# Kernel tuning notes

Measured on AMD Instinct MI355X. Metric: run time of the kernel, lower is better.

Reference implementation:

```python
import jax, jax.numpy as jnp
import numpy as np
import math

D_MODEL = 2048
N_HEADS = 16
D_HEAD = D_MODEL // N_HEADS

def setup_inputs() -> dict:
    key = jax.random.key(0)
    ks = jax.random.split(key, 6)
    B, S, D = 4, 2048, D_MODEL
    scale = 1.0 / math.sqrt(D)
    x  = jax.random.normal(ks[0], (B, S, D), dtype=jnp.float32)
    Wq = jax.random.normal(ks[1], (D, D), dtype=jnp.float32) * scale
    Wk = jax.random.normal(ks[2], (D, D), dtype=jnp.float32) * scale
    Wv = jax.random.normal(ks[3], (D, D), dtype=jnp.float32) * scale
    Wo = jax.random.normal(ks[4], (D, D), dtype=jnp.float32) * scale
    bo = jax.random.normal(ks[5], (D,), dtype=jnp.float32) * 0.01
    return {"x": x, "Wq": Wq, "Wk": Wk, "Wv": Wv, "Wo": Wo, "bo": bo}

def reference(x, Wq, Wk, Wv, Wo, bo):
    B, S, D = x.shape
    H, Dh = N_HEADS, D_HEAD
    # projections (bias=False for q/k/v); torch Linear: y = x @ W^T
    q = (x @ Wq.T).reshape(B, S, H, Dh).transpose(0, 2, 1, 3)  # [B,H,S,Dh]
    k = (x @ Wk.T).reshape(B, S, H, Dh).transpose(0, 2, 1, 3)
    v = (x @ Wv.T).reshape(B, S, H, Dh).transpose(0, 2, 1, 3)
    scores = jnp.einsum('bhqd,bhkd->bhqk', q, k) / math.sqrt(Dh)  # [B,H,S,S]
    causal = jnp.tril(jnp.ones((S, S), dtype=bool))
    scores = jnp.where(causal, scores, -jnp.inf)
    attn = jax.nn.softmax(scores, axis=-1)
    # dropout p=0.0 -> identity (eval)
    out = jnp.einsum('bhqk,bhkd->bhqd', attn, v)  # [B,H,S,Dh]
    out = out.transpose(0, 2, 1, 3).reshape(B, S, D)
    return out @ Wo.T + bo
```

## Files before the change

kernel.cpp:

```cpp
#include <hip/hip_runtime.h>
#include <stdint.h>

#define D_MODEL 2048
#define NH 16
#define DH 128
#define BATCH 4
#define SEQ 2048
#define MTOT (BATCH*SEQ)
#define LDQ 6144

typedef __bf16 bf16x8 __attribute__((ext_vector_type(8)));
typedef float f32x4 __attribute__((ext_vector_type(4)));
typedef short short8 __attribute__((ext_vector_type(8)));

static __device__ __forceinline__ unsigned short f2bf(float f) {
  union { float f; unsigned int u; } v; v.f = f;
  return (unsigned short)((v.u + 0x7FFFu + ((v.u >> 16) & 1u)) >> 16);
}

#define FENCEM() asm volatile("" ::: "memory")
#define GBAR() do { FENCEM(); __builtin_amdgcn_s_barrier(); FENCEM(); } while (0)

__global__ __launch_bounds__(256) void cvt_all_k(const float* __restrict__ x,
                                                 const float* __restrict__ w0, const float* __restrict__ w1,
                                                 const float* __restrict__ w2, const float* __restrict__ w3,
                                                 unsigned short* __restrict__ xo,
                                                 unsigned short* __restrict__ wo_cat,
                                                 unsigned short* __restrict__ wo_o) {
  const size_t WSZ = (size_t)D_MODEL * D_MODEL;
  int id = blockIdx.x;
  const float* src; unsigned short* dst; int lo;
  if (id < 8192) { src = x; dst = xo; lo = id; }
  else {
    int wsel = (id - 8192) >> 11;
    lo = (id - 8192) & 2047;
    switch (wsel) {
      case 0: src = w0; dst = wo_cat; break;
      case 1: src = w1; dst = wo_cat + WSZ; break;
      case 2: src = w2; dst = wo_cat + 2 * WSZ; break;
      default: src = w3; dst = wo_o; break;
    }
  }
  int i = (lo * 256 + threadIdx.x) * 8;
  float4 a = *(const float4*)(src + i);
  float4 b = *(const float4*)(src + i + 4);
  union { unsigned short u[8]; short8 v; } o;
  o.u[0] = f2bf(a.x); o.u[1] = f2bf(a.y); o.u[2] = f2bf(a.z); o.u[3] = f2bf(a.w);
  o.u[4] = f2bf(b.x); o.u[5] = f2bf(b.y); o.u[6] = f2bf(b.z); o.u[7] = f2bf(b.w);
  *(short8*)(dst + i) = o.v;
}

template<bool OUT_BF16, bool ADD_BIAS>
__global__ __launch_bounds__(512, 2) void gemm256(const unsigned short* __restrict__ A,
                                                  const unsigned short* __restrict__ B,
                                                  void* __restrict__ C,
                                                  const float* __restrict__ bias,
                                                  int M, int N, int K) {
  __shared__ __align__(16) unsigned short As[2][256 * 64];
  __shared__ __align__(16) unsigned short Bs[2][256 * 64];

  const int tid = threadIdx.x;
  const int lane = tid & 63;
  const int l15 = lane & 15, l4 = lane >> 4;
  const int wid = tid >> 6;
  const int wr = wid >> 2, wc = wid & 3;

  const int gx = gridDim.x;
  const int id = blockIdx.y * gx + blockIdx.x;
  const int msl = gx >> 2;
  const int nsl = gridDim.y >> 1;
  const int xcd = id & 7;
  const int lid = id >> 3;
  const int bm = (xcd >> 1) * msl + lid / nsl;
  const int bn = (xcd & 1) * nsl + lid % nsl;

  const int NT = K >> 6;

  const int st_r = tid >> 3;
  const int st_c = (tid & 7) ^ (st_r & 7);
  const int st_ld = st_r * 64 + (tid & 7) * 8;

#define STAGE_A(t, h) do { \
  const int _b = (t) & 1; \
  _Pragma("unroll") \
  for (int _i = 0; _i < 2; ++_i) { \
    const unsigned short* _g = A + (size_t)(bm * 256 + (h) * 128 + _i * 64 + st_r) * K + (t) * 64 + st_c * 8; \
    __builtin_amdgcn_global_load_lds((const __attribute__((address_space(1))) void*)_g, \
        (__attribute__((address_space(3))) void*)(&As[_b][(h) * 8192 + _i * 4096 + st_ld]), 16, 0, 0); \
  } \
} while (0)

#define STAGE_B(t, h) do { \
  const int _b = (t) & 1; \
  _Pragma("unroll") \
  for (int _i = 0; _i < 2; ++_i) { \
    const unsigned short* _g = B + (size_t)(bn * 256 + (h) * 128 + _i * 64 + st_r) * K + (t) * 64 + st_c * 8; \
    __builtin_amdgcn_global_load_lds((const __attribute__((address_space(1))) void*)_g, \
        (__attribute__((address_space(3))) void*)(&Bs[_b][(h) * 8192 + _i * 4096 + st_ld]), 16, 0, 0); \
  } \
} while (0)

#define LDA_F(dst, bufb, mh) do { \
  _Pragma("unroll") \
  for (int _mi = 0; _mi < 4; ++_mi) { \
    int _row = wr * 128 + (mh) * 64 + _mi * 16 + l15; \
    _Pragma("unroll") \
    for (int _kk = 0; _kk < 2; ++_kk) \
      dst[_mi][_kk] = *(const bf16x8*)&As[bufb][_row * 64 + ((_kk * 4 + l4) ^ (l15 & 7)) * 8]; \
  } \
} while (0)

#define LDB_F(dst, bufb, nq) do { \
  _Pragma("unroll") \
  for (int _ni = 0; _ni < 2; ++_ni) { \
    int _row = wc * 64 + (nq) * 32 + _ni * 16 + l15; \
    _Pragma("unroll") \
    for (int _kk = 0; _kk < 2; ++_kk) \
      dst[_ni][_kk] = *(const bf16x8*)&Bs[bufb][_row * 64 + ((_kk * 4 + l4) ^ (l15 & 7)) * 8]; \
  } \
} while (0)

#define PHASE_MFMA(MH, NQ, BFR) do { \
  _Pragma("unroll") \
  for (int _mi = 0; _mi < 4; ++_mi) { \
    _Pragma("unroll") \
    for (int _ni = 0; _ni < 2; ++_ni) { \
      acc[(MH) * 4 + _mi][(NQ) * 2 + _ni] = __builtin_amdgcn_mfma_f32_16x16x32_bf16( \
          af[_mi][0], BFR[_ni][0], acc[(MH) * 4 + _mi][(NQ) * 2 + _ni], 0, 0, 0); \
      acc[(MH) * 4 + _mi][(NQ) * 2 + _ni] = __builtin_amdgcn_mfma_f32_16x16x32_bf16( \
          af[_mi][1], BFR[_ni][1], acc[(MH) * 4 + _mi][(NQ) * 2 + _ni], 0, 0, 0); \
    } \
  } \
} while (0)

  f32x4 acc[8][4] = {};

  STAGE_A(0, 0); STAGE_A(0, 1);
  STAGE_B(0, 0); STAGE_B(0, 1);
  if (NT > 1) { STAGE_A(1, 0); STAGE_A(1, 1); }
  if (NT > 1) asm volatile("s_waitcnt vmcnt(4)" ::: "memory");
  else        asm volatile("s_waitcnt vmcnt(0)" ::: "memory");
  GBAR();

  for (int t = 0; t < NT; ++t) {
    const int bufb = t & 1;
    bf16x8 af[4][2], bf0[2][2], bf1[2][2];

    LDA_F(af, bufb, 0);
    LDB_F(bf0, bufb, 0);
    LDB_F(bf1, bufb, 1);
    if (t + 1 < NT) { STAGE_B(t + 1, 0); STAGE_B(t + 1, 1); }
    __builtin_amdgcn_s_setprio(1);
    PHASE_MFMA(0, 0, bf0);
    PHASE_MFMA(0, 1, bf1);
    __builtin_amdgcn_s_setprio(0);

    LDA_F(af, bufb, 1);
    asm volatile("s_waitcnt lgkmcnt(0)" ::: "memory");
    GBAR();

    if (t + 2 < NT) { STAGE_A(t + 2, 0); STAGE_A(t + 2, 1); }
    __builtin_amdgcn_s_setprio(1);
    PHASE_MFMA(1, 1, bf1);
    PHASE_MFMA(1, 0, bf0);
    __builtin_amdgcn_s_setprio(0);
    if (t + 2 < NT) asm volatile("s_waitcnt vmcnt(4)" ::: "memory");
    else            asm volatile("s_waitcnt vmcnt(0)" ::: "memory");
    GBAR();
  }

  const int row0 = bm * 256 + wr * 128;
  const int col0 = bn * 256 + wc * 64;
#pragma unroll
  for (int mi = 0; mi < 8; ++mi) {
#pragma unroll
    for (int ni = 0; ni < 4; ++ni) {
      int col = col0 + ni * 16 + l15;
#pragma unroll
      for (int r = 0; r < 4; ++r) {
        int row = row0 + mi * 16 + l4 * 4 + r;
        float v = acc[mi][ni][r];
        if (ADD_BIAS) v += bias[col];
        if (OUT_BF16)
          ((unsigned short*)C)[(size_t)row * N + col] = f2bf(v);
        else
          ((float*)C)[(size_t)row * N + col] = v;
      }
    }
  }
#undef STAGE_A
#undef STAGE_B
#undef LDA_F
#undef LDB_F
#undef PHASE_MFMA
}

__global__ __launch_bounds__(256, 2) void attn_k(const unsigned short* __restrict__ Qp,
                                                 const unsigned short* __restrict__ Kp,
                                                 const unsigned short* __restrict__ Vp,
                                                 unsigned short* __restrict__ O) {
  __shared__ __align__(16) unsigned short Ks[2][64 * 128];
  __shared__ __align__(16) unsigned short Vt[2][128 * 64];
  __shared__ __align__(16) unsigned int   Pl[4][32 * 32];

  const int tid = threadIdx.x;
  const int lane = tid & 63;
  const int l15 = lane & 15, l4 = lane >> 4;
  const int w = tid >> 6;

  const int idx = blockIdx.y * gridDim.x + blockIdx.x;
  const int x8 = idx & 7, j = idx >> 3;
  const int bh = x8 * 8 + (j & 7);
  const int qt = 15 - (j >> 3);
  const int b = bh >> 4, h = bh & 15;

  const size_t baseI = (size_t)b * SEQ * LDQ + (size_t)h * DH;
  const size_t baseO = (size_t)b * SEQ * D_MODEL + (size_t)h * DH;
  const int qw = qt * 128 + w * 32;

  bf16x8 qf[2][4];
#pragma unroll
  for (int qg = 0; qg < 2; ++qg) {
    const unsigned short* qptr = Qp + baseI + (size_t)(qw + qg * 16 + l15) * LDQ;
#pragma unroll
    for (int kk = 0; kk < 4; ++kk)
      qf[qg][kk] = *(const bf16x8*)(qptr + kk * 32 + l4 * 8);
  }

  f32x4 acc[2][8] = {};
  float m_run[2] = {-3.4028235e38f, -3.4028235e38f};
  float lp[2] = {0.f, 0.f};
  const float SC = 0.12751743f;

  short8 vreg[4];
  const int nkt = 2 * qt + 2;

  const int vkp0 = tid >> 4, vch0 = tid & 15;
  const int vkp1 = (tid + 256) >> 4, vch1 = vch0;

#pragma unroll
  for (int it = 0; it < 4; ++it) {
    int c = tid + it * 256;
    int key = c >> 4, pos = c & 15;
    int gchunk = pos ^ (key & 7);
    const unsigned short* ga = Kp + baseI + (size_t)key * LDQ + gchunk * 8;
    __builtin_amdgcn_global_load_lds((const __attribute__((address_space(1))) void*)ga,
                                     (__attribute__((address_space(3))) void*)(&Ks[0][c * 8]),
                                     16, 0, 0);
  }
  FENCEM();
  {
    const unsigned short* gv0 = Vp + baseI + (size_t)(2 * vkp0) * LDQ + vch0 * 8;
    vreg[0] = *(const short8*)(gv0);
    vreg[1] = *(const short8*)(gv0 + LDQ);
    const unsigned short* gv1 = Vp + baseI + (size_t)(2 * vkp1) * LDQ + vch1 * 8;
    vreg[2] = *(const short8*)(gv1);
    vreg[3] = *(const short8*)(gv1 + LDQ);
  }

  for (int kt = 0; kt < nkt; ++kt) {
    const int cur = kt & 1;
    const int kv0 = kt * 64;
    const bool act = (kv0 <= qw + 31);

    asm volatile("s_waitcnt vmcnt(4)" ::: "memory");
    GBAR();

    f32x4 sacc[2][4] = {};
    if (act) {
      __builtin_amdgcn_s_setprio(1);
#pragma unroll
      for (int st = 0; st < 4; ++st) {
        int key = st * 16 + l15;
#pragma unroll
        for (int kk = 0; kk < 4; ++kk) {
          bf16x8 kf = *(const bf16x8*)&Ks[cur][key * 128 + ((kk * 32 + l4 * 8) ^ ((key & 7) << 3))];
          sacc[0][st] = __builtin_amdgcn_mfma_f32_16x16x32_bf16(kf, qf[0][kk], sacc[0][st], 0, 0, 0);
          sacc[1][st] = __builtin_amdgcn_mfma_f32_16x16x32_bf16(kf, qf[1][kk], sacc[1][st], 0, 0, 0);
        }
      }
      __builtin_amdgcn_s_setprio(0);
    }
    FENCEM();

    if (kt + 1 < nkt) {
      const int kn0 = kv0 + 64;
      const int nb = cur ^ 1;
#pragma unroll
      for (int it = 0; it < 4; ++it) {
        int c = tid + it * 256;
        int key = c >> 4, pos = c & 15;
        int gchunk = pos ^ (key & 7);
        const unsigned short* ga = Kp + baseI + (size_t)(kn0 + key) * LDQ + gchunk * 8;
        __builtin_amdgcn_global_load_lds((const __attribute__((address_space(1))) void*)ga,
                                         (__attribute__((address_space(3))) void*)(&Ks[nb][c * 8]),
                                         16, 0, 0);
      }
      asm volatile("s_waitcnt vmcnt(4)" ::: "memory");
    } else {
      asm volatile("s_waitcnt vmcnt(0)" ::: "memory");
    }

#pragma unroll
    for (int i = 0; i < 2; ++i) {
      int kp = i ? vkp1 : vkp0;
      int ch = i ? vch1 : vch0;
      union { short8 v; unsigned short u[8]; } ua, ub;
      ua.v = vreg[2 * i]; ub.v = vreg[2 * i + 1];
#pragma unroll
      for (int j2 = 0; j2 < 8; ++j2) {
        int dh = ch * 8 + j2;
        int sv = (ch ^ j2) & 7;
        unsigned val = (unsigned)ua.u[j2] | ((unsigned)ub.u[j2] << 16);
        *(unsigned int*)&Vt[cur][dh * 64 + ((2 * kp) ^ (sv << 3))] = val;
      }
    }
    if (kt + 1 < nkt) {
      const int kn0 = kv0 + 64;
      const unsigned short* gv0 = Vp + baseI + (size_t)(kn0 + 2 * vkp0) * LDQ + vch0 * 8;
      vreg[0] = *(const short8*)(gv0);
      vreg[1] = *(const short8*)(gv0 + LDQ);
      const unsigned short* gv1 = Vp + baseI + (size_t)(kn0 + 2 * vkp1) * LDQ + vch1 * 8;
      vreg[2] = *(const short8*)(gv1);
      vreg[3] = *(const short8*)(gv1 + LDQ);
    }
    __syncthreads();

    if (act) {
      const bool tail = (kv0 + 63 > qw);
      float tmax[2];
#pragma unroll
      for (int qg = 0; qg < 2; ++qg) {
        if (tail) {
          int q = qw + qg * 16 + l15;
#pragma unroll
          for (int st = 0; st < 4; ++st)
#pragma unroll
            for (int r = 0; r < 4; ++r) {
              int key = kv0 + st * 16 + l4 * 4 + r;
              if (key > q) sacc[qg][st][r] = -3.0e38f;
            }
        }
        float a0 = fmaxf(fmaxf(sacc[qg][0][0], sacc[qg][0][1]), fmaxf(sacc[qg][0][2], sacc[qg][0][3]));
        float a1 = fmaxf(fmaxf(sacc[qg][1][0], sacc[qg][1][1]), fmaxf(sacc[qg][1][2], sacc[qg][1][3]));
        float a2 = fmaxf(fmaxf(sacc[qg][2][0], sacc[qg][2][1]), fmaxf(sacc[qg][2][2], sacc[qg][2][3]));
        float a3 = fmaxf(fmaxf(sacc[qg][3][0], sacc[qg][3][1]), fmaxf(sacc[qg][3][2], sacc[qg][3][3]));
        float t = fmaxf(fmaxf(a0, a1), fmaxf(a2, a3));
        t = fmaxf(t, __shfl_xor(t, 16));
        t = fmaxf(t, __shfl_xor(t, 32));
        tmax[qg] = t;
      }
      bool grow = (tmax[0] > m_run[0] + 8.f) || (tmax[1] > m_run[1] + 8.f);
      if (__any(grow)) {
#pragma unroll
        for (int qg = 0; qg < 2; ++qg) {
          float nm = fmaxf(m_run[qg], tmax[qg]);
          float scl = __builtin_amdgcn_exp2f((m_run[qg] - nm) * SC);
          m_run[qg] = nm;
          lp[qg] *= scl;
#pragma unroll
          for (int r = 0; r < 4; ++r) {
            float srow = __shfl(scl, l4 * 4 + r);
#pragma unroll
            for (int df = 0; df < 8; ++df) acc[qg][df][r] *= srow;
          }
        }
      }
#pragma unroll
      for (int qg = 0; qg < 2; ++qg) {
        int q = qg * 16 + l15;
        float ps = 0.f;
#pragma unroll
        for (int st = 0; st < 4; ++st) {
          float p0 = __builtin_amdgcn_exp2f((sacc[qg][st][0] - m_run[qg]) * SC);
          float p1 = __builtin_amdgcn_exp2f((sacc[qg][st][1] - m_run[qg]) * SC);
          float p2 = __builtin_amdgcn_exp2f((sacc[qg][st][2] - m_run[qg]) * SC);
          float p3 = __builtin_amdgcn_exp2f((sacc[qg][st][3] - m_run[qg]) * SC);
          ps += (p0 + p1) + (p2 + p3);
          unsigned w0 = (unsigned)f2bf(p0) | ((unsigned)f2bf(p1) << 16);
          unsigned w1 = (unsigned)f2bf(p2) | ((unsigned)f2bf(p3) << 16);
          int kw0 = st * 8 + l4 * 2;
          Pl[w][q * 32 + (kw0 ^ ((q & 7) << 2))] = w0;
          Pl[w][q * 32 + ((kw0 + 1) ^ ((q & 7) << 2))] = w1;
        }
        lp[qg] += ps;
      }
      __builtin_amdgcn_s_setprio(1);
#pragma unroll
      for (int ks2 = 0; ks2 < 2; ++ks2) {
        int kwb = ks2 * 16 + l4 * 4;
        bf16x8 pa0 = *(const bf16x8*)&Pl[w][l15 * 32 + (kwb ^ ((l15 & 7) << 2))];
        bf16x8 pa1 = *(const bf16x8*)&Pl[w][(16 + l15) * 32 + (kwb ^ ((l15 & 7) << 2))];
#pragma unroll
        for (int df = 0; df < 8; ++df) {
          int dh = df * 16 + l15;
          int sv = ((dh >> 3) ^ dh) & 7;
          bf16x8 vb = *(const bf16x8*)&Vt[cur][dh * 64 + ((ks2 * 32 + l4 * 8) ^ (sv << 3))];
          acc[0][df] = __builtin_amdgcn_mfma_f32_16x16x32_bf16(pa0, vb, acc[0][df], 0, 0, 0);
          acc[1][df] = __builtin_amdgcn_mfma_f32_16x16x32_bf16(pa1, vb, acc[1][df], 0, 0, 0);
        }
      }
      __builtin_amdgcn_s_setprio(0);
    }
  }

#pragma unroll
  for (int qg = 0; qg < 2; ++qg) {
    float t = lp[qg];
    t += __shfl_xor(t, 16);
    t += __shfl_xor(t, 32);
    float linv = 1.0f / t;
#pragma unroll
    for (int r = 0; r < 4; ++r) {
      float lrow = __shfl(linv, l4 * 4 + r);
      int row = qw + qg * 16 + l4 * 4 + r;
#pragma unroll
      for (int df = 0; df < 8; ++df)
        O[baseO + (size_t)row * D_MODEL + df * 16 + l15] = f2bf(acc[qg][df][r] * lrow);
    }
  }
}

extern "C" void kernel_launch(void* const* d_in, const int* in_sizes, int n_in,
                              void* d_out, int out_size, void* d_ws, size_t ws_size,
                              hipStream_t stream) {
  const float* x  = (const float*)d_in[0];
  const float* Wq = (const float*)d_in[1];
  const float* Wk = (const float*)d_in[2];
  const float* Wv = (const float*)d_in[3];
  const float* Wo = (const float*)d_in[4];
  const float* bo = (const float*)d_in[5];
  float* out = (float*)d_out;

  unsigned short* ws = (unsigned short*)d_ws;
  const size_t XSZ = (size_t)MTOT * D_MODEL;
  const size_t WSZ = (size_t)D_MODEL * D_MODEL;
  unsigned short* xb   = ws;
  unsigned short* Wcat = xb + XSZ;
  unsigned short* Wob  = Wcat + 3 * WSZ;
  unsigned short* QKV  = Wob + WSZ;
  unsigned short* AOb  = xb;

  cvt_all_k<<<16384, 256, 0, stream>>>(x, Wq, Wk, Wv, Wo, xb, Wcat, Wob);

  dim3 gq(MTOT / 256, LDQ / 256);
  gemm256<true, false><<<gq, 512, 0, stream>>>(xb, Wcat, QKV, nullptr, MTOT, LDQ, D_MODEL);

  dim3 ga(SEQ / 128, BATCH * NH);
  attn_k<<<ga, 256, 0, stream>>>(QKV, QKV + 2048, QKV + 4096, AOb);

  dim3 gg(MTOT / 256, D_MODEL / 256);
  gemm256<false, true><<<gg, 512, 0, stream>>>(AOb, Wob, out, bo, MTOT, D_MODEL, D_MODEL);
}
```

Baseline: 388.6 us.

## Restructure GEMM into quadrant-wise eight-barrier pipeline with per-half staging

Changes the GEMM warp-to-tile mapping so each wave covers interleaved quadrants (64x32 pieces spread across both 128-row and 128-col halves) instead of a contiguous 128x64 block. The K-loop is split into four quadrant MFMA phases, each separated by barriers and each overlapping one half-tile global-to-LDS stage, in the style of an 8-wave ping-pong schedule. The goal is finer-grained overlap of loads with MFMA, at the cost of many more barriers per iteration and more complex vmcnt accounting. Bias is also hoisted out of the inner row loop in the epilogue.

```diff
diff --git a/kernel.cpp b/kernel.cpp
--- a/kernel.cpp
+++ b/kernel.cpp
@@ -100,44 +100,45 @@
   } \
 } while (0)
 
-#define LDA_F(dst, bufb, mh) do { \
+#define LDA_Q(dst, bufb, qm) do { \
   _Pragma("unroll") \
   for (int _mi = 0; _mi < 4; ++_mi) { \
-    int _row = wr * 128 + (mh) * 64 + _mi * 16 + l15; \
+    int _row = (qm) * 128 + wr * 64 + _mi * 16 + l15; \
     _Pragma("unroll") \
     for (int _kk = 0; _kk < 2; ++_kk) \
       dst[_mi][_kk] = *(const bf16x8*)&As[bufb][_row * 64 + ((_kk * 4 + l4) ^ (l15 & 7)) * 8]; \
   } \
 } while (0)
 
-#define LDB_F(dst, bufb, nq) do { \
+#define LDB_Q(dst, bufb, qn) do { \
   _Pragma("unroll") \
   for (int _ni = 0; _ni < 2; ++_ni) { \
-    int _row = wc * 64 + (nq) * 32 + _ni * 16 + l15; \
+    int _row = (qn) * 128 + wc * 32 + _ni * 16 + l15; \
     _Pragma("unroll") \
     for (int _kk = 0; _kk < 2; ++_kk) \
       dst[_ni][_kk] = *(const bf16x8*)&Bs[bufb][_row * 64 + ((_kk * 4 + l4) ^ (l15 & 7)) * 8]; \
   } \
 } while (0)
 
-#define PHASE_MFMA(MH, NQ, BFR) do { \
+#define QMFMA(QM, QN, BFR) do { \
+  __builtin_amdgcn_s_setprio(1); \
   _Pragma("unroll") \
   for (int _mi = 0; _mi < 4; ++_mi) { \
     _Pragma("unroll") \
     for (int _ni = 0; _ni < 2; ++_ni) { \
-      acc[(MH) * 4 + _mi][(NQ) * 2 + _ni] = __builtin_amdgcn_mfma_f32_16x16x32_bf16( \
-          af[_mi][0], BFR[_ni][0], acc[(MH) * 4 + _mi][(NQ) * 2 + _ni], 0, 0, 0); \
-      acc[(MH) * 4 + _mi][(NQ) * 2 + _ni] = __builtin_amdgcn_mfma_f32_16x16x32_bf16( \
-          af[_mi][1], BFR[_ni][1], acc[(MH) * 4 + _mi][(NQ) * 2 + _ni], 0, 0, 0); \
+      acc[(QM) * 4 + _mi][(QN) * 2 + _ni] = __builtin_amdgcn_mfma_f32_16x16x32_bf16( \
+          af[_mi][0], BFR[_ni][0], acc[(QM) * 4 + _mi][(QN) * 2 + _ni], 0, 0, 0); \
+      acc[(QM) * 4 + _mi][(QN) * 2 + _ni] = __builtin_amdgcn_mfma_f32_16x16x32_bf16( \
+          af[_mi][1], BFR[_ni][1], acc[(QM) * 4 + _mi][(QN) * 2 + _ni], 0, 0, 0); \
     } \
   } \
+  __builtin_amdgcn_s_setprio(0); \
 } while (0)
 
   f32x4 acc[8][4] = {};
 
-  STAGE_A(0, 0); STAGE_A(0, 1);
-  STAGE_B(0, 0); STAGE_B(0, 1);
-  if (NT > 1) { STAGE_A(1, 0); STAGE_A(1, 1); }
+  STAGE_A(0, 0); STAGE_A(0, 1); STAGE_B(0, 0); STAGE_B(0, 1);
+  if (NT > 1) { STAGE_A(1, 0); STAGE_B(1, 1); }
   if (NT > 1) asm volatile("s_waitcnt vmcnt(4)" ::: "memory");
   else        asm volatile("s_waitcnt vmcnt(0)" ::: "memory");
   GBAR();
@@ -146,53 +147,68 @@
     const int bufb = t & 1;
     bf16x8 af[4][2], bf0[2][2], bf1[2][2];
 
-    LDA_F(af, bufb, 0);
-    LDB_F(bf0, bufb, 0);
-    LDB_F(bf1, bufb, 1);
-    if (t + 1 < NT) { STAGE_B(t + 1, 0); STAGE_B(t + 1, 1); }
-    __builtin_amdgcn_s_setprio(1);
-    PHASE_MFMA(0, 0, bf0);
-    PHASE_MFMA(0, 1, bf1);
-    __builtin_amdgcn_s_setprio(0);
-
-    LDA_F(af, bufb, 1);
+    LDA_Q(af, bufb, 0);
+    LDB_Q(bf0, bufb, 0);
+    if (t + 1 < NT) STAGE_A(t + 1, 1);
+    asm volatile("s_waitcnt lgkmcnt(8)" ::: "memory");
+    GBAR();
     asm volatile("s_waitcnt lgkmcnt(0)" ::: "memory");
-    GBAR();
-
-    if (t + 2 < NT) { STAGE_A(t + 2, 0); STAGE_A(t + 2, 1); }
-    __builtin_amdgcn_s_setprio(1);
-    PHASE_MFMA(1, 1, bf1);
-    PHASE_MFMA(1, 0, bf0);
-    __builtin_amdgcn_s_setprio(0);
+    QMFMA(0, 0, bf0);
+    GBAR();
+
+    LDB_Q(bf1, bufb, 1);
+    if (t + 1 < NT) STAGE_B(t + 1, 0);
+    GBAR();
+    asm volatile("s_waitcnt lgkmcnt(0)" ::: "memory");
+    QMFMA(0, 1, bf1);
+    GBAR();
+
+    LDA_Q(af, bufb, 1);
+    if (t + 2 < NT) STAGE_A(t + 2, 0);
+    GBAR();
+    asm volatile("s_waitcnt lgkmcnt(0)" ::: "memory");
+    QMFMA(1, 1, bf1);
+    GBAR();
+
+    if (t + 2 < NT) STAGE_B(t + 2, 1);
+    GBAR();
+    QMFMA(1, 0, bf0);
     if (t + 2 < NT) asm volatile("s_waitcnt vmcnt(4)" ::: "memory");
     else            asm volatile("s_waitcnt vmcnt(0)" ::: "memory");
     GBAR();
   }
 
-  const int row0 = bm * 256 + wr * 128;
-  const int col0 = bn * 256 + wc * 64;
-#pragma unroll
-  for (int mi = 0; mi < 8; ++mi) {
-#pragma unroll
-    for (int ni = 0; ni < 4; ++ni) {
-      int col = col0 + ni * 16 + l15;
-#pragma unroll
-      for (int r = 0; r < 4; ++r) {
-        int row = row0 + mi * 16 + l4 * 4 + r;
-        float v = acc[mi][ni][r];
-        if (ADD_BIAS) v += bias[col];
-        if (OUT_BF16)
-          ((unsigned short*)C)[(size_t)row * N + col] = f2bf(v);
-        else
-          ((float*)C)[(size_t)row * N + col] = v;
+  const int row0 = bm * 256 + wr * 64;
+  const int col0 = bn * 256 + wc * 32;
+#pragma unroll
+  for (int qm = 0; qm < 2; ++qm) {
+#pragma unroll
+    for (int mi = 0; mi < 4; ++mi) {
+#pragma unroll
+      for (int qn = 0; qn < 2; ++qn) {
+#pragma unroll
+        for (int ni = 0; ni < 2; ++ni) {
+          int col = col0 + qn * 128 + ni * 16 + l15;
+          float bv = ADD_BIAS ? bias[col] : 0.f;
+#pragma unroll
+          for (int r = 0; r < 4; ++r) {
+            int row = row0 + qm * 128 + mi * 16 + l4 * 4 + r;
+            float v = acc[qm * 4 + mi][qn * 2 + ni][r];
+            if (ADD_BIAS) v += bv;
+            if (OUT_BF16)
+              ((unsigned short*)C)[(size_t)row * N + col] = f2bf(v);
+            else
+              ((float*)C)[(size_t)row * N + col] = v;
+          }
+        }
       }
     }
   }
 #undef STAGE_A
 #undef STAGE_B
-#undef LDA_F
-#undef LDB_F
-#undef PHASE_MFMA
+#undef LDA_Q
+#undef LDB_Q
+#undef QMFMA
 }
 
 __global__ __launch_bounds__(256, 2) void attn_k(const unsigned short* __restrict__ Qp,
```

After: 398.4 us. +2.5%, slower.
